# Optimization experiments

Hardware: AMD Instinct MI355X
Metric: run time of the kernel (lower is better)

## Reference

```python
import jax, jax.numpy as jnp
import numpy as np

TEMPERATURE = 1.0
N_ITER = 3
B, N_PATTERNS, N_NEURONS = 4096, 8192, 1024


def setup_inputs() -> dict:
    key = jax.random.key(0)
    kx, kp = jax.random.split(key)
    x = jax.random.normal(kx, (B, N_NEURONS), dtype=jnp.float32)
    # patterns initialized as tanh(randn * initial_variance) in the original module
    patterns = jnp.tanh(jax.random.normal(kp, (N_PATTERNS, N_NEURONS), dtype=jnp.float32) * 0.1)
    return {"x": x, "patterns": patterns}


def reference(x, patterns):
    # Iterative Hopfield update: x <- softmax(T * x @ P^T) @ P, repeated N_ITER times.
    def body(carry, _):
        scores = TEMPERATURE * jnp.einsum('bn,pn->bp', carry, patterns)  # [B, P]
        new_x = jnp.einsum('bp,pn->bn', jax.nn.softmax(scores, axis=1), patterns)  # [B, N]
        return new_x, None
    x, _ = jax.lax.scan(body, x, None, length=N_ITER)
    return x
```

## Files before the change

kernel.cpp:

```cpp
#include <hip/hip_runtime.h>
#include <hip/hip_fp16.h>
#include <stdint.h>

#define B_ROWS 4096
#define N_PAT  8192
#define N_NEU  1024

typedef _Float16 f16x8 __attribute__((ext_vector_type(8)));
typedef _Float16 f16x4 __attribute__((ext_vector_type(4)));
typedef float    f32x4 __attribute__((ext_vector_type(4)));

__device__ __forceinline__ f32x4 mfma16(f16x8 a, f16x8 b, f32x4 c) {
  return __builtin_amdgcn_mfma_f32_16x16x32_f16(a, b, c, 0, 0, 0);
}

__global__ __launch_bounds__(256) void convert_f32_f16(
    const float* __restrict__ in, _Float16* __restrict__ out, int n4) {
  int idx    = blockIdx.x * 256 + threadIdx.x;
  int stride = gridDim.x * 256;
  for (int i = idx; i < n4; i += stride) {
    float4 v = reinterpret_cast<const float4*>(in)[i];
    f16x4 h  = { (_Float16)v.x, (_Float16)v.y, (_Float16)v.z, (_Float16)v.w };
    reinterpret_cast<f16x4*>(out)[i] = h;
  }
}

__global__ __launch_bounds__(256) void transpose_f32_f16(
    const float* __restrict__ in, _Float16* __restrict__ out, int rows, int cols) {
  __shared__ float tile[32][33];
  int c0 = blockIdx.x * 32, r0 = blockIdx.y * 32;
  int tx = threadIdx.x, ty = threadIdx.y;
  #pragma unroll
  for (int i = 0; i < 32; i += 8)
    tile[ty + i][tx] = in[(size_t)(r0 + ty + i) * cols + c0 + tx];
  __syncthreads();
  #pragma unroll
  for (int i = 0; i < 32; i += 8)
    out[(size_t)(c0 + ty + i) * rows + r0 + tx] = (_Float16)tile[tx][ty + i];
}

__device__ __forceinline__ void gload_lds16(const _Float16* g, _Float16* l) {
  __builtin_amdgcn_global_load_lds(
      (const __attribute__((address_space(1))) uint32_t*)g,
      (__attribute__((address_space(3))) uint32_t*)l, 16, 0, 0);
}

template <typename OUT_T>
__global__ __launch_bounds__(512, 2) void gemm_x(
    const _Float16* __restrict__ A, const _Float16* __restrict__ Bt,
    OUT_T* __restrict__ C, int M, int N, int K, int KS) {
  __shared__ _Float16 lds[2][2][256 * 64];
  const int t    = threadIdx.x;
  const int lane = t & 63;
  const int w    = t >> 6;
  const int wr   = w >> 2;
  const int wc   = w & 3;
  const int m0   = blockIdx.x * 256;
  const int n0   = blockIdx.y * 256;
  const int k0   = blockIdx.z * KS;

  const int srow  = w * 8 + (lane >> 3);
  const int sgran = ((lane & 7) ^ ((lane >> 3) & 7)) * 8;
  const _Float16* sA = A  + (size_t)(m0 + srow) * K + sgran + k0;
  const _Float16* sB = Bt + (size_t)(n0 + srow) * K + sgran + k0;
  const size_t rj = (size_t)64 * K;
  const int ldst  = w * 512;

  const int lrow = lane & 15;
  const int kg   = lane >> 4;
  const int NT   = KS >> 6;

  f32x4 acc[8][4] = {};

  auto stageAh = [&](int slot, int kt, int h) {
    gload_lds16(sA + (size_t)(2 * h)     * rj + kt, &lds[slot][0][(2 * h)     * 4096 + ldst]);
    gload_lds16(sA + (size_t)(2 * h + 1) * rj + kt, &lds[slot][0][(2 * h + 1) * 4096 + ldst]);
  };
  auto stageBh = [&](int slot, int kt, int h) {
    gload_lds16(sB + (size_t)(2 * h)     * rj + kt, &lds[slot][1][(2 * h)     * 4096 + ldst]);
    gload_lds16(sB + (size_t)(2 * h + 1) * rj + kt, &lds[slot][1][(2 * h + 1) * 4096 + ldst]);
  };

#define READ_AF(dst, MI0)                                                                   \
  { const int ar0 = wr * 128 + (MI0) * 16 + lrow;                                           \
    dst[0] = *reinterpret_cast<const f16x8*>(&As[ar0 * 64 + (((kg) ^ (ar0 & 7)) * 8)]);     \
    dst[1] = *reinterpret_cast<const f16x8*>(&As[ar0 * 64 + (((4 + kg) ^ (ar0 & 7)) * 8)]); \
    const int ar1 = ar0 + 16;                                                               \
    dst[2] = *reinterpret_cast<const f16x8*>(&As[ar1 * 64 + (((kg) ^ (ar1 & 7)) * 8)]);     \
    dst[3] = *reinterpret_cast<const f16x8*>(&As[ar1 * 64 + (((4 + kg) ^ (ar1 & 7)) * 8)]); }

#define MFMA_Q(MI0, src)                                                      \
  { __builtin_amdgcn_s_setprio(1);                                            \
    _Pragma("unroll")                                                         \
    for (int ni = 0; ni < 4; ++ni) {                                          \
      acc[MI0][ni]       = mfma16(src[0], bf[ni][0], acc[MI0][ni]);           \
      acc[MI0][ni]       = mfma16(src[1], bf[ni][1], acc[MI0][ni]);           \
      acc[(MI0) + 1][ni] = mfma16(src[2], bf[ni][0], acc[(MI0) + 1][ni]);     \
      acc[(MI0) + 1][ni] = mfma16(src[3], bf[ni][1], acc[(MI0) + 1][ni]);     \
    }                                                                         \
    __builtin_amdgcn_s_setprio(0); }

#define BAR() asm volatile("s_barrier" ::: "memory")

  stageBh(0, 0, 0);  stageBh(0, 0, 1);
  stageAh(0, 0, 0);  stageAh(0, 0, 1);
  stageBh(1, 64, 0); stageBh(1, 64, 1);

  for (int tt = 0; tt < NT; ++tt) {
    const int s = tt & 1;
    if (tt + 1 < NT) asm volatile("s_waitcnt vmcnt(4)" ::: "memory");
    else             asm volatile("s_waitcnt vmcnt(0)" ::: "memory");
    BAR();

    const _Float16* As = lds[s][0];
    const _Float16* Bs = lds[s][1];
    const int ktA  = (tt + 1) << 6;
    const int ktB  = (tt + 2) << 6;
    const bool pA  = (tt + 1 < NT);
    const bool pB  = (tt + 2 < NT);

    f16x8 bf[4][2], afP[4], afQ[4];
    #pragma unroll
    for (int ni = 0; ni < 4; ++ni) {
      const int br = wc * 64 + ni * 16 + lrow;
      bf[ni][0] = *reinterpret_cast<const f16x8*>(&Bs[br * 64 + (((kg) ^ (br & 7)) * 8)]);
      bf[ni][1] = *reinterpret_cast<const f16x8*>(&Bs[br * 64 + (((4 + kg) ^ (br & 7)) * 8)]);
    }
    READ_AF(afP, 0)

    if (pA) stageAh(s ^ 1, ktA, 0);
    READ_AF(afQ, 2)
    BAR();
    MFMA_Q(0, afP)
    if (pA) stageAh(s ^ 1, ktA, 1);
    READ_AF(afP, 4)
    BAR();
    MFMA_Q(2, afQ)
    if (pB) stageBh(s, ktB, 0);
    READ_AF(afQ, 6)
    BAR();
    MFMA_Q(4, afP)
    if (pB) stageBh(s, ktB, 1);
    BAR();
    MFMA_Q(6, afQ)
  }

  OUT_T* Cz = C + (size_t)blockIdx.z * M * N;
  const int crow = (lane >> 4) * 4;
  const int ccol = lane & 15;
  #pragma unroll
  for (int mi = 0; mi < 8; ++mi) {
    #pragma unroll
    for (int ni = 0; ni < 4; ++ni) {
      #pragma unroll
      for (int r = 0; r < 4; ++r) {
        int row = m0 + wr * 128 + mi * 16 + crow + r;
        int col = n0 + wc * 64 + ni * 16 + ccol;
        Cz[(size_t)row * N + col] = (OUT_T)acc[mi][ni][r];
      }
    }
  }
#undef READ_AF
#undef MFMA_Q
#undef BAR
}

template <typename OUT_T, int SPLIT>
__global__ __launch_bounds__(256) void reduce_partials(
    const float* __restrict__ Cp, OUT_T* __restrict__ out, int n4, int stride4) {
  int idx    = blockIdx.x * 256 + threadIdx.x;
  int stride = gridDim.x * 256;
  for (int i = idx; i < n4; i += stride) {
    float4 a = reinterpret_cast<const float4*>(Cp)[i];
    #pragma unroll
    for (int s = 1; s < SPLIT; ++s) {
      float4 b = reinterpret_cast<const float4*>(Cp)[(size_t)s * stride4 + i];
      a.x += b.x; a.y += b.y; a.z += b.z; a.w += b.w;
    }
    if constexpr (sizeof(OUT_T) == 2) {
      f16x4 h = { (_Float16)a.x, (_Float16)a.y, (_Float16)a.z, (_Float16)a.w };
      reinterpret_cast<f16x4*>(out)[i] = h;
    } else {
      reinterpret_cast<float4*>(out)[i] = a;
    }
  }
}

__global__ __launch_bounds__(256) void softmax_rows(_Float16* __restrict__ S, int N) {
  const int t = threadIdx.x;
  f16x8* pv = reinterpret_cast<f16x8*>(S + (size_t)blockIdx.x * N);
  float v[32];
  float m = -3.0e38f;
  #pragma unroll
  for (int i = 0; i < 4; ++i) {
    f16x8 h = pv[i * 256 + t];
    #pragma unroll
    for (int e = 0; e < 8; ++e) {
      float f = (float)h[e];
      v[i * 8 + e] = f;
      m = fmaxf(m, f);
    }
  }
  #pragma unroll
  for (int o = 32; o; o >>= 1) m = fmaxf(m, __shfl_xor(m, o));
  __shared__ float redm[4];
  if ((t & 63) == 0) redm[t >> 6] = m;
  __syncthreads();
  m = fmaxf(fmaxf(redm[0], redm[1]), fmaxf(redm[2], redm[3]));

  float s = 0.f;
  #pragma unroll
  for (int i = 0; i < 32; ++i) { v[i] = __expf(v[i] - m); s += v[i]; }
  #pragma unroll
  for (int o = 32; o; o >>= 1) s += __shfl_xor(s, o);
  __shared__ float reds[4];
  if ((t & 63) == 0) reds[t >> 6] = s;
  __syncthreads();
  s = reds[0] + reds[1] + reds[2] + reds[3];
  const float inv = 1.0f / s;

  #pragma unroll
  for (int i = 0; i < 4; ++i) {
    f16x8 h;
    #pragma unroll
    for (int e = 0; e < 8; ++e) h[e] = (_Float16)(v[i * 8 + e] * inv);
    pv[i * 256 + t] = h;
  }
}

extern "C" void kernel_launch(void* const* d_in, const int* in_sizes, int n_in,
                              void* d_out, int out_size, void* d_ws, size_t ws_size,
                              hipStream_t stream) {
  const float* x        = (const float*)d_in[0];
  const float* patterns = (const float*)d_in[1];
  float* out            = (float*)d_out;
  char* ws = (char*)d_ws;

  _Float16* Xb   = (_Float16*)(ws);
  _Float16* Pb   = (_Float16*)(ws + ((size_t)8  << 20));
  _Float16* PbT  = (_Float16*)(ws + ((size_t)24 << 20));
  _Float16* S    = (_Float16*)(ws + ((size_t)40 << 20));
  float*    part = (float*)   (ws + ((size_t)104 << 20));

  const size_t base = (size_t)104 << 20;
  const int split = (ws_size >= base + ((size_t)64 << 20)) ? 4
                  : (ws_size >= base + ((size_t)32 << 20)) ? 2 : 1;

  convert_f32_f16<<<dim3(1024), dim3(256), 0, stream>>>(x, Xb, (B_ROWS * N_NEU) / 4);
  convert_f32_f16<<<dim3(2048), dim3(256), 0, stream>>>(patterns, Pb, (N_PAT * N_NEU) / 4);
  transpose_f32_f16<<<dim3(N_NEU / 32, N_PAT / 32), dim3(32, 8), 0, stream>>>(patterns, PbT, N_PAT, N_NEU);

  const int n4 = (B_ROWS * N_NEU) / 4;
  const int stride4 = n4;

  for (int it = 0; it < 3; ++it) {
    gemm_x<_Float16><<<dim3(B_ROWS / 256, N_PAT / 256, 1), dim3(512), 0, stream>>>(
        Xb, Pb, S, B_ROWS, N_PAT, N_NEU, N_NEU);
    softmax_rows<<<dim3(B_ROWS), dim3(256), 0, stream>>>(S, N_PAT);

    if (split > 1) {
      gemm_x<float><<<dim3(B_ROWS / 256, N_NEU / 256, split), dim3(512), 0, stream>>>(
          S, PbT, part, B_ROWS, N_NEU, N_PAT, N_PAT / split);
      if (it < 2) {
        if (split == 4)
          reduce_partials<_Float16, 4><<<dim3(2048), dim3(256), 0, stream>>>(part, Xb, n4, stride4);
        else
          reduce_partials<_Float16, 2><<<dim3(2048), dim3(256), 0, stream>>>(part, Xb, n4, stride4);
      } else {
        if (split == 4)
          reduce_partials<float, 4><<<dim3(2048), dim3(256), 0, stream>>>(part, out, n4, stride4);
        else
          reduce_partials<float, 2><<<dim3(2048), dim3(256), 0, stream>>>(part, out, n4, stride4);
      }
    } else {
      gemm_x<float><<<dim3(B_ROWS / 256, N_NEU / 256, 1), dim3(512), 0, stream>>>(
          S, PbT, part, B_ROWS, N_NEU, N_PAT, N_PAT);
      if (it < 2)
        reduce_partials<_Float16, 1><<<dim3(2048), dim3(256), 0, stream>>>(part, Xb, n4, stride4);
      else
        reduce_partials<float, 1><<<dim3(2048), dim3(256), 0, stream>>>(part, out, n4, stride4);
    }
  }
}
```

Measured before the change: 519.6 us.

## Restructure GEMM main loop into two phases and fuse pattern conversion kernels

The GEMM inner loop changes from four interleaved phases with five barriers per K-tile to two halves with two barriers. All next-tile A loads are issued up front, and B loads for the tile after next are issued mid-tile. Separately, the f16 copy and f16 transpose of the patterns are produced by one kernel, so the f32 patterns are read once instead of twice. The coarser schedule cuts barrier overhead but gives less fine-grained overlap of LDS reads, global-to-LDS loads and MFMA work.

```diff
diff --git a/kernel.cpp b/kernel.cpp
--- a/kernel.cpp
+++ b/kernel.cpp
@@ -25,18 +25,22 @@
   }
 }
 
-__global__ __launch_bounds__(256) void transpose_f32_f16(
-    const float* __restrict__ in, _Float16* __restrict__ out, int rows, int cols) {
+__global__ __launch_bounds__(256) void prep_patterns(
+    const float* __restrict__ in, _Float16* __restrict__ pb,
+    _Float16* __restrict__ pbt, int rows, int cols) {
   __shared__ float tile[32][33];
   int c0 = blockIdx.x * 32, r0 = blockIdx.y * 32;
   int tx = threadIdx.x, ty = threadIdx.y;
   #pragma unroll
+  for (int i = 0; i < 32; i += 8) {
+    float v = in[(size_t)(r0 + ty + i) * cols + c0 + tx];
+    tile[ty + i][tx] = v;
+    pb[(size_t)(r0 + ty + i) * cols + c0 + tx] = (_Float16)v;
+  }
+  __syncthreads();
+  #pragma unroll
   for (int i = 0; i < 32; i += 8)
-    tile[ty + i][tx] = in[(size_t)(r0 + ty + i) * cols + c0 + tx];
-  __syncthreads();
-  #pragma unroll
-  for (int i = 0; i < 32; i += 8)
-    out[(size_t)(c0 + ty + i) * rows + r0 + tx] = (_Float16)tile[tx][ty + i];
+    pbt[(size_t)(c0 + ty + i) * rows + r0 + tx] = (_Float16)tile[tx][ty + i];
 }
 
 __device__ __forceinline__ void gload_lds16(const _Float16* g, _Float16* l) {
@@ -81,22 +85,20 @@
     gload_lds16(sB + (size_t)(2 * h + 1) * rj + kt, &lds[slot][1][(2 * h + 1) * 4096 + ldst]);
   };
 
-#define READ_AF(dst, MI0)                                                                   \
+#define READ_AF2(dst, MI0)                                                                  \
   { const int ar0 = wr * 128 + (MI0) * 16 + lrow;                                           \
-    dst[0] = *reinterpret_cast<const f16x8*>(&As[ar0 * 64 + (((kg) ^ (ar0 & 7)) * 8)]);     \
-    dst[1] = *reinterpret_cast<const f16x8*>(&As[ar0 * 64 + (((4 + kg) ^ (ar0 & 7)) * 8)]); \
-    const int ar1 = ar0 + 16;                                                               \
-    dst[2] = *reinterpret_cast<const f16x8*>(&As[ar1 * 64 + (((kg) ^ (ar1 & 7)) * 8)]);     \
-    dst[3] = *reinterpret_cast<const f16x8*>(&As[ar1 * 64 + (((4 + kg) ^ (ar1 & 7)) * 8)]); }
-
-#define MFMA_Q(MI0, src)                                                      \
+    dst[(MI0) & 3][0] = *reinterpret_cast<const f16x8*>(&As[ar0 * 64 + (((kg) ^ (ar0 & 7)) * 8)]);     \
+    dst[(MI0) & 3][1] = *reinterpret_cast<const f16x8*>(&As[ar0 * 64 + (((4 + kg) ^ (ar0 & 7)) * 8)]); }
+
+#define MFMA_HALF(MI0, src)                                                   \
   { __builtin_amdgcn_s_setprio(1);                                            \
     _Pragma("unroll")                                                         \
-    for (int ni = 0; ni < 4; ++ni) {                                          \
-      acc[MI0][ni]       = mfma16(src[0], bf[ni][0], acc[MI0][ni]);           \
-      acc[MI0][ni]       = mfma16(src[1], bf[ni][1], acc[MI0][ni]);           \
-      acc[(MI0) + 1][ni] = mfma16(src[2], bf[ni][0], acc[(MI0) + 1][ni]);     \
-      acc[(MI0) + 1][ni] = mfma16(src[3], bf[ni][1], acc[(MI0) + 1][ni]);     \
+    for (int mi = 0; mi < 4; ++mi) {                                          \
+      _Pragma("unroll")                                                       \
+      for (int ni = 0; ni < 4; ++ni) {                                        \
+        acc[(MI0) + mi][ni] = mfma16(src[mi][0], bf[ni][0], acc[(MI0) + mi][ni]); \
+        acc[(MI0) + mi][ni] = mfma16(src[mi][1], bf[ni][1], acc[(MI0) + mi][ni]); \
+      }                                                                       \
     }                                                                         \
     __builtin_amdgcn_s_setprio(0); }
 
@@ -116,33 +118,23 @@
     const _Float16* Bs = lds[s][1];
     const int ktA  = (tt + 1) << 6;
     const int ktB  = (tt + 2) << 6;
-    const bool pA  = (tt + 1 < NT);
-    const bool pB  = (tt + 2 < NT);
-
-    f16x8 bf[4][2], afP[4], afQ[4];
+
+    if (tt + 1 < NT) { stageAh(s ^ 1, ktA, 0); stageAh(s ^ 1, ktA, 1); }
+    f16x8 bf[4][2], af[4][2];
     #pragma unroll
     for (int ni = 0; ni < 4; ++ni) {
       const int br = wc * 64 + ni * 16 + lrow;
       bf[ni][0] = *reinterpret_cast<const f16x8*>(&Bs[br * 64 + (((kg) ^ (br & 7)) * 8)]);
       bf[ni][1] = *reinterpret_cast<const f16x8*>(&Bs[br * 64 + (((4 + kg) ^ (br & 7)) * 8)]);
     }
-    READ_AF(afP, 0)
-
-    if (pA) stageAh(s ^ 1, ktA, 0);
-    READ_AF(afQ, 2)
+    READ_AF2(af, 0) READ_AF2(af, 1) READ_AF2(af, 2) READ_AF2(af, 3)
+    MFMA_HALF(0, af)
+
     BAR();
-    MFMA_Q(0, afP)
-    if (pA) stageAh(s ^ 1, ktA, 1);
-    READ_AF(afP, 4)
-    BAR();
-    MFMA_Q(2, afQ)
-    if (pB) stageBh(s, ktB, 0);
-    READ_AF(afQ, 6)
-    BAR();
-    MFMA_Q(4, afP)
-    if (pB) stageBh(s, ktB, 1);
-    BAR();
-    MFMA_Q(6, afQ)
+
+    if (tt + 2 < NT) { stageBh(s, ktB, 0); stageBh(s, ktB, 1); }
+    READ_AF2(af, 4) READ_AF2(af, 5) READ_AF2(af, 6) READ_AF2(af, 7)
+    MFMA_HALF(4, af)
   }
 
   OUT_T* Cz = C + (size_t)blockIdx.z * M * N;
@@ -160,8 +152,8 @@
       }
     }
   }
-#undef READ_AF
-#undef MFMA_Q
+#undef READ_AF2
+#undef MFMA_HALF
 #undef BAR
 }
 
@@ -247,8 +239,8 @@
                   : (ws_size >= base + ((size_t)32 << 20)) ? 2 : 1;
 
   convert_f32_f16<<<dim3(1024), dim3(256), 0, stream>>>(x, Xb, (B_ROWS * N_NEU) / 4);
-  convert_f32_f16<<<dim3(2048), dim3(256), 0, stream>>>(patterns, Pb, (N_PAT * N_NEU) / 4);
-  transpose_f32_f16<<<dim3(N_NEU / 32, N_PAT / 32), dim3(32, 8), 0, stream>>>(patterns, PbT, N_PAT, N_NEU);
+  prep_patterns<<<dim3(N_NEU / 32, N_PAT / 32), dim3(32, 8), 0, stream>>>(
+      patterns, Pb, PbT, N_PAT, N_NEU);
 
   const int n4 = (B_ROWS * N_NEU) / 4;
   const int stride4 = n4;
```

After: 520.5 us. Within noise of the previous version (+0.2%).
